# Kernel optimization log

Hardware: AMD Instinct MI355X
Metric: run time of the kernel (lower is better)

## Reference

```python
import jax, jax.numpy as jnp
import numpy as np

N_NODES = 100000


def _gcn_norm(edge_index, num_nodes):
    # Add self-loops, then symmetric normalization D^-1/2 A D^-1/2 (PyG gcn_norm).
    loops = jnp.arange(num_nodes, dtype=edge_index.dtype)
    src = jnp.concatenate([edge_index[0], loops])
    dst = jnp.concatenate([edge_index[1], loops])
    ew = jnp.ones(src.shape[0], dtype=jnp.float32)
    deg = jax.ops.segment_sum(ew, dst, num_segments=num_nodes)
    dinv = jnp.where(deg > 0, jax.lax.rsqrt(deg), 0.0)
    norm = dinv[src] * ew * dinv[dst]
    return src, dst, norm


def _prop_gcn_conv(x, W, b, src, dst, norm, num_nodes, prop_nums):
    # PropGCNConv: linear transform once, then prop_nums hops of normalized
    # sparse propagation (gather from src, scale, scatter-add to dst), + bias.
    x = x @ W
    for _ in range(prop_nums):
        msgs = x[src] * norm[:, None]              # [E, d]
        x = jax.ops.segment_sum(msgs, dst, num_segments=num_nodes)
    return x + b


def setup_inputs() -> dict:
    key = jax.random.key(0)
    k1, k2, k3, k4 = jax.random.split(key, 4)
    in_dim, hid_dim, num_classes = 128, 64, 40
    n_edges = 800000
    x = jax.random.normal(k1, (N_NODES, in_dim), dtype=jnp.float32)
    W0 = jax.random.normal(k2, (in_dim, hid_dim), dtype=jnp.float32) * (1.0 / np.sqrt(in_dim))
    b0 = jnp.zeros((hid_dim,), dtype=jnp.float32)
    Wc = jax.random.normal(k3, (hid_dim, num_classes), dtype=jnp.float32) * (1.0 / np.sqrt(hid_dim))
    bc = jnp.zeros((num_classes,), dtype=jnp.float32)
    edge_index = jax.random.randint(k4, (2, n_edges), 0, N_NODES, dtype=jnp.int64)
    return {"x": x, "W0": W0, "b0": b0, "Wc": Wc, "bc": bc,
            "edge_index": edge_index, "prop_nums": 30}


def reference(x, W0, b0, Wc, bc, edge_index, prop_nums):
    n = x.shape[0]
    src, dst, norm = _gcn_norm(edge_index, n)
    # feat_bottleneck: conv -> relu -> dropout (eval mode -> identity)
    h = _prop_gcn_conv(x, W0, b0, src, dst, norm, n, prop_nums)
    h = jax.nn.relu(h)
    # feat_classifier: single-hop PropGCNConv
    out = _prop_gcn_conv(h, Wc, bc, src, dst, norm, n, 1)
    return out
```

## Files before the change

### kernel.cpp

```cpp
#include <hip/hip_runtime.h>

#define NN  100000
#define NE  800000
#define NNZ 900000
#define IN_DIM 128
#define HID 64
#define NC  40
#define HOPS 30

typedef _Float16 half8 __attribute__((ext_vector_type(8)));


__global__ void count_edges_k(const int* __restrict__ dst, int* __restrict__ cnt) {
    int e = blockIdx.x * blockDim.x + threadIdx.x;
    if (e < NE) atomicAdd(&cnt[dst[e]], 1);
}

__global__ void dinv_k(const int* __restrict__ cnt, float* __restrict__ dinv) {
    int i = blockIdx.x * blockDim.x + threadIdx.x;
    if (i < NN) dinv[i] = rsqrtf((float)(cnt[i] + 1));
}

__global__ void scan_blocks_k(const int* __restrict__ cnt, int* __restrict__ rp,
                              int* __restrict__ partials) {
    __shared__ int s[256];
    int tid = threadIdx.x;
    int i = blockIdx.x * 256 + tid;
    int v = (i < NN) ? (cnt[i] + 1) : 0;
    s[tid] = v;
    __syncthreads();
    for (int off = 1; off < 256; off <<= 1) {
        int t = (tid >= off) ? s[tid - off] : 0;
        __syncthreads();
        s[tid] += t;
        __syncthreads();
    }
    if (i < NN) rp[i] = s[tid] - v;
    if (tid == 255) partials[blockIdx.x] = s[255];
}

__global__ void scan_partials_k(int* __restrict__ partials, int nblk) {
    __shared__ int s[512];
    int tid = threadIdx.x;
    int v = (tid < nblk) ? partials[tid] : 0;
    s[tid] = v;
    __syncthreads();
    for (int off = 1; off < 512; off <<= 1) {
        int t = (tid >= off) ? s[tid - off] : 0;
        __syncthreads();
        s[tid] += t;
        __syncthreads();
    }
    if (tid < nblk) partials[tid] = s[tid] - v;
}

__global__ void add_offsets_k(int* __restrict__ rp, const int* __restrict__ partials) {
    int i = blockIdx.x * 256 + threadIdx.x;
    if (i < NN) rp[i] += partials[blockIdx.x];
    if (i == 0) rp[NN] = NNZ;
}

__global__ void fill_csr_k(const int* __restrict__ src, const int* __restrict__ dst,
                           const float* __restrict__ dinv, const int* __restrict__ rp,
                           int* __restrict__ cnt, int2* __restrict__ cv) {
    int e = blockIdx.x * blockDim.x + threadIdx.x;
    if (e >= NNZ) return;
    int pos;
    int2 p;
    if (e < NE) {
        int s = src[e], d = dst[e];
        int old = atomicAdd(&cnt[d], -1);
        pos = rp[d] + old - 1;
        p.x = s;
        p.y = __float_as_int(dinv[s] * dinv[d]);
    } else {
        int i = e - NE;
        pos = rp[i + 1] - 1;
        p.x = i;
        p.y = __float_as_int(dinv[i] * dinv[i]);
    }
    cv[pos] = p;
}


__global__ void __launch_bounds__(256) gemm1_k(const float* __restrict__ x,
                                               const float* __restrict__ W,
                                               _Float16* __restrict__ out) {
    int t = threadIdx.x;
    int cq = __builtin_amdgcn_readfirstlane(t >> 6);
    int node = blockIdx.x * 64 + (t & 63);
    int nc = node < NN ? node : NN - 1;
    const float4* xr = (const float4*)(x + (size_t)nc * IN_DIM);
    const float* Wq = W + cq * 16;
    float acc[16];
#pragma unroll
    for (int c = 0; c < 16; ++c) acc[c] = 0.f;
#pragma unroll 4
    for (int k4 = 0; k4 < IN_DIM / 4; ++k4) {
        float4 xv = xr[k4];
#pragma unroll
        for (int kk = 0; kk < 4; ++kk) {
            float xs = (kk == 0) ? xv.x : (kk == 1) ? xv.y : (kk == 2) ? xv.z : xv.w;
            const float4* wr = (const float4*)(Wq + (k4 * 4 + kk) * HID);
#pragma unroll
            for (int c4 = 0; c4 < 4; ++c4) {
                float4 wv = wr[c4];
                acc[c4 * 4 + 0] = fmaf(xs, wv.x, acc[c4 * 4 + 0]);
                acc[c4 * 4 + 1] = fmaf(xs, wv.y, acc[c4 * 4 + 1]);
                acc[c4 * 4 + 2] = fmaf(xs, wv.z, acc[c4 * 4 + 2]);
                acc[c4 * 4 + 3] = fmaf(xs, wv.w, acc[c4 * 4 + 3]);
            }
        }
    }
    if (node < NN) {
        half8* o = (half8*)(out + (size_t)node * HID + cq * 16);
        half8 r0, r1;
#pragma unroll
        for (int j = 0; j < 8; ++j) {
            r0[j] = (_Float16)acc[j];
            r1[j] = (_Float16)acc[j + 8];
        }
        o[0] = r0;
        o[1] = r1;
    }
}

__global__ void prop64_k(const _Float16* __restrict__ xin, _Float16* __restrict__ xout,
                         const int* __restrict__ rp, const int2* __restrict__ cv) {
    int wid  = threadIdx.x >> 6;
    int lane = threadIdx.x & 63;
    int n    = lane >> 5;
    int s    = (lane >> 3) & 3;
    int f    = lane & 7;
    int node = blockIdx.x * 8 + wid * 2 + n;
    int beg = rp[node], end = rp[node + 1];
    const half8* x8 = (const half8*)xin;
    float a0 = 0.f, a1 = 0.f, a2 = 0.f, a3 = 0.f, a4 = 0.f, a5 = 0.f, a6 = 0.f, a7 = 0.f;
    for (int e = beg + s; e < end; e += 16) {
        int  e1 = e + 4,  e2 = e + 8,  e3 = e + 12;
        bool p1 = e1 < end, p2 = e2 < end, p3 = e3 < end;
        int2 q0 = cv[e];
        int2 q1 = cv[p1 ? e1 : beg];
        int2 q2 = cv[p2 ? e2 : beg];
        int2 q3 = cv[p3 ? e3 : beg];
        float v0 = __int_as_float(q0.y);
        float v1 = p1 ? __int_as_float(q1.y) : 0.f;
        float v2 = p2 ? __int_as_float(q2.y) : 0.f;
        float v3 = p3 ? __int_as_float(q3.y) : 0.f;
        half8 x0 = x8[(size_t)q0.x * 8 + f];
        half8 x1 = x8[(size_t)q1.x * 8 + f];
        half8 x2 = x8[(size_t)q2.x * 8 + f];
        half8 x3 = x8[(size_t)q3.x * 8 + f];
        a0 += v0 * (float)x0[0] + v1 * (float)x1[0] + v2 * (float)x2[0] + v3 * (float)x3[0];
        a1 += v0 * (float)x0[1] + v1 * (float)x1[1] + v2 * (float)x2[1] + v3 * (float)x3[1];
        a2 += v0 * (float)x0[2] + v1 * (float)x1[2] + v2 * (float)x2[2] + v3 * (float)x3[2];
        a3 += v0 * (float)x0[3] + v1 * (float)x1[3] + v2 * (float)x2[3] + v3 * (float)x3[3];
        a4 += v0 * (float)x0[4] + v1 * (float)x1[4] + v2 * (float)x2[4] + v3 * (float)x3[4];
        a5 += v0 * (float)x0[5] + v1 * (float)x1[5] + v2 * (float)x2[5] + v3 * (float)x3[5];
        a6 += v0 * (float)x0[6] + v1 * (float)x1[6] + v2 * (float)x2[6] + v3 * (float)x3[6];
        a7 += v0 * (float)x0[7] + v1 * (float)x1[7] + v2 * (float)x2[7] + v3 * (float)x3[7];
    }
#pragma unroll
    for (int m = 8; m <= 16; m <<= 1) {
        a0 += __shfl_xor(a0, m); a1 += __shfl_xor(a1, m);
        a2 += __shfl_xor(a2, m); a3 += __shfl_xor(a3, m);
        a4 += __shfl_xor(a4, m); a5 += __shfl_xor(a5, m);
        a6 += __shfl_xor(a6, m); a7 += __shfl_xor(a7, m);
    }
    if (s == 0) {
        half8 r;
        r[0] = (_Float16)a0; r[1] = (_Float16)a1; r[2] = (_Float16)a2; r[3] = (_Float16)a3;
        r[4] = (_Float16)a4; r[5] = (_Float16)a5; r[6] = (_Float16)a6; r[7] = (_Float16)a7;
        ((half8*)xout)[(size_t)node * 8 + f] = r;
    }
}

__global__ void __launch_bounds__(256, 4) gemm2_k(const _Float16* __restrict__ h,
                                                  const float* __restrict__ b0,
                                                  const float* __restrict__ Wc,
                                                  _Float16* __restrict__ g) {
    __shared__ float Wcs[HID * NC];
    __shared__ float b0s[HID];
    int t = threadIdx.x;
    for (int i = t; i < HID * NC / 4; i += 256)
        ((float4*)Wcs)[i] = ((const float4*)Wc)[i];
    if (t < HID) b0s[t] = b0[t];
    __syncthreads();
    int node = blockIdx.x * 256 + t;
    if (node >= NN) return;
    const half8* hr = (const half8*)(h + (size_t)node * HID);
    float acc[NC];
#pragma unroll
    for (int c = 0; c < NC; ++c) acc[c] = 0.f;
#pragma unroll
    for (int j = 0; j < 8; ++j) {
        half8 hv = hr[j];
#pragma unroll
        for (int m = 0; m < 8; ++m) {
            int k = j * 8 + m;
            float fv = fmaxf((float)hv[m] + b0s[k], 0.f);
            const float4* wr = (const float4*)(Wcs + k * NC);
#pragma unroll
            for (int c4 = 0; c4 < NC / 4; ++c4) {
                float4 wv = wr[c4];
                acc[c4 * 4 + 0] = fmaf(fv, wv.x, acc[c4 * 4 + 0]);
                acc[c4 * 4 + 1] = fmaf(fv, wv.y, acc[c4 * 4 + 1]);
                acc[c4 * 4 + 2] = fmaf(fv, wv.z, acc[c4 * 4 + 2]);
                acc[c4 * 4 + 3] = fmaf(fv, wv.w, acc[c4 * 4 + 3]);
            }
        }
    }
    half8* go = (half8*)(g + (size_t)node * NC);
#pragma unroll
    for (int j = 0; j < 5; ++j) {
        half8 r;
#pragma unroll
        for (int m = 0; m < 8; ++m) r[m] = (_Float16)acc[j * 8 + m];
        go[j] = r;
    }
}

__global__ void prop40_k(const _Float16* __restrict__ g, float* __restrict__ out,
                         const int* __restrict__ rp, const int2* __restrict__ cv,
                         const float* __restrict__ bc) {
    int t = blockIdx.x * 256 + threadIdx.x;
    int node = t >> 6;
    int lane = threadIdx.x & 63;
    int s = lane >> 3;
    int f = lane & 7;
    int beg = rp[node], end = rp[node + 1];
    const half8* g8 = (const half8*)g;
    bool act = f < 5;
    float a0 = 0.f, a1 = 0.f, a2 = 0.f, a3 = 0.f, a4 = 0.f, a5 = 0.f, a6 = 0.f, a7 = 0.f;
    for (int e = beg + s; e < end; e += 16) {
        int  e1 = e + 8;
        bool p1 = e1 < end;
        int2 q0 = cv[e];
        int2 q1 = cv[p1 ? e1 : beg];
        float v0 = __int_as_float(q0.y);
        float v1 = p1 ? __int_as_float(q1.y) : 0.f;
        if (act) {
            half8 x0 = g8[(size_t)q0.x * 5 + f];
            half8 x1 = g8[(size_t)q1.x * 5 + f];
            a0 += v0 * (float)x0[0] + v1 * (float)x1[0];
            a1 += v0 * (float)x0[1] + v1 * (float)x1[1];
            a2 += v0 * (float)x0[2] + v1 * (float)x1[2];
            a3 += v0 * (float)x0[3] + v1 * (float)x1[3];
            a4 += v0 * (float)x0[4] + v1 * (float)x1[4];
            a5 += v0 * (float)x0[5] + v1 * (float)x1[5];
            a6 += v0 * (float)x0[6] + v1 * (float)x1[6];
            a7 += v0 * (float)x0[7] + v1 * (float)x1[7];
        }
    }
#pragma unroll
    for (int m = 8; m <= 32; m <<= 1) {
        a0 += __shfl_xor(a0, m); a1 += __shfl_xor(a1, m);
        a2 += __shfl_xor(a2, m); a3 += __shfl_xor(a3, m);
        a4 += __shfl_xor(a4, m); a5 += __shfl_xor(a5, m);
        a6 += __shfl_xor(a6, m); a7 += __shfl_xor(a7, m);
    }
    if (s == 0 && act) {
        float* o = out + (size_t)node * NC + f * 8;
        o[0] = a0 + bc[f * 8 + 0];
        o[1] = a1 + bc[f * 8 + 1];
        o[2] = a2 + bc[f * 8 + 2];
        o[3] = a3 + bc[f * 8 + 3];
        o[4] = a4 + bc[f * 8 + 4];
        o[5] = a5 + bc[f * 8 + 5];
        o[6] = a6 + bc[f * 8 + 6];
        o[7] = a7 + bc[f * 8 + 7];
    }
}


extern "C" void kernel_launch(void* const* d_in, const int* in_sizes, int n_in,
                              void* d_out, int out_size, void* d_ws, size_t ws_size,
                              hipStream_t stream) {
    const float* x  = (const float*)d_in[0];
    const float* W0 = (const float*)d_in[1];
    const float* b0 = (const float*)d_in[2];
    const float* Wc = (const float*)d_in[3];
    const float* bc = (const float*)d_in[4];
    const int*   ei = (const int*)d_in[5];
    const int* src = ei;
    const int* dst = ei + NE;

    char* ws = (char*)d_ws;
    size_t off = 0;
    auto alloc = [&](size_t bytes) -> void* {
        void* p = ws + off;
        off = (off + bytes + 255) & ~(size_t)255;
        return p;
    };
    float* dinv     = (float*)alloc((size_t)NN * 4);
    int*   rp       = (int*)  alloc((size_t)(NN + 1) * 4);
    int*   cnt      = (int*)  alloc((size_t)NN * 4);
    int*   partials = (int*)  alloc(512 * 4);
    int2*  cvp      = (int2*) alloc((size_t)NNZ * 8);
    _Float16* XA    = (_Float16*)alloc((size_t)NN * HID * 2);
    _Float16* XB    = (_Float16*)alloc((size_t)NN * HID * 2);
    _Float16* G     = (_Float16*)alloc((size_t)NN * NC * 2);

    const int nblk_n = (NN + 255) / 256;

    hipMemsetAsync(cnt, 0, (size_t)NN * 4, stream);
    count_edges_k<<<(NE + 255) / 256, 256, 0, stream>>>(dst, cnt);
    dinv_k       <<<nblk_n, 256, 0, stream>>>(cnt, dinv);
    scan_blocks_k<<<nblk_n, 256, 0, stream>>>(cnt, rp, partials);
    scan_partials_k<<<1, 512, 0, stream>>>(partials, nblk_n);
    add_offsets_k<<<nblk_n, 256, 0, stream>>>(rp, partials);
    fill_csr_k   <<<(NNZ + 255) / 256, 256, 0, stream>>>(src, dst, dinv, rp, cnt, cvp);

    gemm1_k<<<(NN + 63) / 64, 256, 0, stream>>>(x, W0, XA);

    _Float16* a = XA;
    _Float16* b = XB;
    for (int hop = 0; hop < HOPS; ++hop) {
        prop64_k<<<NN / 8, 256, 0, stream>>>(a, b, rp, cvp);
        _Float16* tmp = a; a = b; b = tmp;
    }

    gemm2_k<<<nblk_n, 256, 0, stream>>>(a, b0, Wc, G);
    prop40_k<<<NN * HID / 256, 256, 0, stream>>>(G, (float*)d_out, rp, cvp, bc);
}
```

Baseline: 829.9 us.

## Split features into 16-wide slabs and fold GCN norm into per-node scales

Features are now stored as four column slabs of 16 halves each, with every slab contiguous over all nodes. The propagation kernel gathers from one slab per block, so the working set of each gather is about a quarter of the full feature matrix and fits more easily in cache. The symmetric normalization is rewritten as a pre-scale by D^-1/2, then unweighted neighbor sums rescaled by 1/deg each hop, with D^-1/2 on the final hop. This lets the CSR store only column indices instead of (index, weight) pairs. Nontemporal loads and stores and a block-index swizzle are also added. The trade-offs are more launched blocks that each re-read the row pointers and indices per slab, and a different rounding path in fp16.

```diff
diff --git a/kernel.cpp b/kernel.cpp
--- a/kernel.cpp
+++ b/kernel.cpp
@@ -7,6 +7,8 @@
 #define HID 64
 #define NC  40
 #define HOPS 30
+#define QF  16
+#define PROP_GRID (8 * 1563)
 
 typedef _Float16 half8 __attribute__((ext_vector_type(8)));
 
@@ -16,9 +18,15 @@
     if (e < NE) atomicAdd(&cnt[dst[e]], 1);
 }
 
-__global__ void dinv_k(const int* __restrict__ cnt, float* __restrict__ dinv) {
+__global__ void dinv_k(const int* __restrict__ cnt, float* __restrict__ dinv,
+                       float* __restrict__ dinv2) {
     int i = blockIdx.x * blockDim.x + threadIdx.x;
-    if (i < NN) dinv[i] = rsqrtf((float)(cnt[i] + 1));
+    if (i < NN) {
+        float deg = (float)(cnt[i] + 1);
+        float dv = rsqrtf(deg);
+        dinv[i] = dv;
+        dinv2[i] = 1.0f / deg;
+    }
 }
 
 __global__ void scan_blocks_k(const int* __restrict__ cnt, int* __restrict__ rp,
@@ -61,30 +69,24 @@
 }
 
 __global__ void fill_csr_k(const int* __restrict__ src, const int* __restrict__ dst,
-                           const float* __restrict__ dinv, const int* __restrict__ rp,
-                           int* __restrict__ cnt, int2* __restrict__ cv) {
+                           const int* __restrict__ rp, int* __restrict__ cnt,
+                           int* __restrict__ col) {
     int e = blockIdx.x * blockDim.x + threadIdx.x;
     if (e >= NNZ) return;
-    int pos;
-    int2 p;
     if (e < NE) {
-        int s = src[e], d = dst[e];
+        int d = dst[e];
         int old = atomicAdd(&cnt[d], -1);
-        pos = rp[d] + old - 1;
-        p.x = s;
-        p.y = __float_as_int(dinv[s] * dinv[d]);
+        col[rp[d] + old - 1] = src[e];
     } else {
         int i = e - NE;
-        pos = rp[i + 1] - 1;
-        p.x = i;
-        p.y = __float_as_int(dinv[i] * dinv[i]);
-    }
-    cv[pos] = p;
+        col[rp[i + 1] - 1] = i;
+    }
 }
 
 
 __global__ void __launch_bounds__(256) gemm1_k(const float* __restrict__ x,
                                                const float* __restrict__ W,
+                                               const float* __restrict__ dinv,
                                                _Float16* __restrict__ out) {
     int t = threadIdx.x;
     int cq = __builtin_amdgcn_readfirstlane(t >> 6);
@@ -113,65 +115,72 @@
         }
     }
     if (node < NN) {
-        half8* o = (half8*)(out + (size_t)node * HID + cq * 16);
+        float dv = dinv[node];
+        half8* o = (half8*)out + ((size_t)cq * NN + node) * 2;
         half8 r0, r1;
 #pragma unroll
         for (int j = 0; j < 8; ++j) {
-            r0[j] = (_Float16)acc[j];
-            r1[j] = (_Float16)acc[j + 8];
+            r0[j] = (_Float16)(acc[j] * dv);
+            r1[j] = (_Float16)(acc[j + 8] * dv);
         }
         o[0] = r0;
         o[1] = r1;
     }
 }
 
-__global__ void prop64_k(const _Float16* __restrict__ xin, _Float16* __restrict__ xout,
-                         const int* __restrict__ rp, const int2* __restrict__ cv) {
+__global__ void __launch_bounds__(256) prop16_k(const _Float16* __restrict__ yin,
+                                                _Float16* __restrict__ yout,
+                                                const int* __restrict__ rp,
+                                                const int* __restrict__ col,
+                                                const float* __restrict__ wsc) {
+    int b = blockIdx.x;
+    int q = (b & 7) >> 1;
+    int g = ((b >> 3) << 1) | (b & 1);
     int wid  = threadIdx.x >> 6;
     int lane = threadIdx.x & 63;
-    int n    = lane >> 5;
-    int s    = (lane >> 3) & 3;
-    int f    = lane & 7;
-    int node = blockIdx.x * 8 + wid * 2 + n;
-    int beg = rp[node], end = rp[node + 1];
-    const half8* x8 = (const half8*)xin;
-    float a0 = 0.f, a1 = 0.f, a2 = 0.f, a3 = 0.f, a4 = 0.f, a5 = 0.f, a6 = 0.f, a7 = 0.f;
-    for (int e = beg + s; e < end; e += 16) {
-        int  e1 = e + 4,  e2 = e + 8,  e3 = e + 12;
-        bool p1 = e1 < end, p2 = e2 < end, p3 = e3 < end;
-        int2 q0 = cv[e];
-        int2 q1 = cv[p1 ? e1 : beg];
-        int2 q2 = cv[p2 ? e2 : beg];
-        int2 q3 = cv[p3 ? e3 : beg];
-        float v0 = __int_as_float(q0.y);
-        float v1 = p1 ? __int_as_float(q1.y) : 0.f;
-        float v2 = p2 ? __int_as_float(q2.y) : 0.f;
-        float v3 = p3 ? __int_as_float(q3.y) : 0.f;
-        half8 x0 = x8[(size_t)q0.x * 8 + f];
-        half8 x1 = x8[(size_t)q1.x * 8 + f];
-        half8 x2 = x8[(size_t)q2.x * 8 + f];
-        half8 x3 = x8[(size_t)q3.x * 8 + f];
-        a0 += v0 * (float)x0[0] + v1 * (float)x1[0] + v2 * (float)x2[0] + v3 * (float)x3[0];
-        a1 += v0 * (float)x0[1] + v1 * (float)x1[1] + v2 * (float)x2[1] + v3 * (float)x3[1];
-        a2 += v0 * (float)x0[2] + v1 * (float)x1[2] + v2 * (float)x2[2] + v3 * (float)x3[2];
-        a3 += v0 * (float)x0[3] + v1 * (float)x1[3] + v2 * (float)x2[3] + v3 * (float)x3[3];
-        a4 += v0 * (float)x0[4] + v1 * (float)x1[4] + v2 * (float)x2[4] + v3 * (float)x3[4];
-        a5 += v0 * (float)x0[5] + v1 * (float)x1[5] + v2 * (float)x2[5] + v3 * (float)x3[5];
-        a6 += v0 * (float)x0[6] + v1 * (float)x1[6] + v2 * (float)x2[6] + v3 * (float)x3[6];
-        a7 += v0 * (float)x0[7] + v1 * (float)x1[7] + v2 * (float)x2[7] + v3 * (float)x3[7];
-    }
-#pragma unroll
-    for (int m = 8; m <= 16; m <<= 1) {
+    int n = lane >> 3;
+    int s = (lane >> 1) & 3;
+    int f = lane & 1;
+    int node = g * 32 + wid * 8 + n;
+    if (node >= NN) node = NN - 1;
+    int beg = __builtin_nontemporal_load(rp + node);
+    int end = __builtin_nontemporal_load(rp + node + 1);
+    const half8* x8 = (const half8*)yin + (size_t)q * NN * 2;
+    float a0 = 0.f, a1 = 0.f, a2 = 0.f, a3 = 0.f,
+          a4 = 0.f, a5 = 0.f, a6 = 0.f, a7 = 0.f;
+    for (int e = beg + s; e < end; e += 8) {
+        int  e1 = e + 4;
+        bool p1 = e1 < end;
+        int c0 = __builtin_nontemporal_load(col + e);
+        int c1 = __builtin_nontemporal_load(col + (p1 ? e1 : e));
+        float w1 = p1 ? 1.f : 0.f;
+        half8 xa = x8[c0 * 2 + f];
+        half8 xb = x8[c1 * 2 + f];
+        a0 += (float)xa[0]; a0 = fmaf(w1, (float)xb[0], a0);
+        a1 += (float)xa[1]; a1 = fmaf(w1, (float)xb[1], a1);
+        a2 += (float)xa[2]; a2 = fmaf(w1, (float)xb[2], a2);
+        a3 += (float)xa[3]; a3 = fmaf(w1, (float)xb[3], a3);
+        a4 += (float)xa[4]; a4 = fmaf(w1, (float)xb[4], a4);
+        a5 += (float)xa[5]; a5 = fmaf(w1, (float)xb[5], a5);
+        a6 += (float)xa[6]; a6 = fmaf(w1, (float)xb[6], a6);
+        a7 += (float)xa[7]; a7 = fmaf(w1, (float)xb[7], a7);
+    }
+#pragma unroll
+    for (int m = 2; m <= 4; m <<= 1) {
         a0 += __shfl_xor(a0, m); a1 += __shfl_xor(a1, m);
         a2 += __shfl_xor(a2, m); a3 += __shfl_xor(a3, m);
         a4 += __shfl_xor(a4, m); a5 += __shfl_xor(a5, m);
         a6 += __shfl_xor(a6, m); a7 += __shfl_xor(a7, m);
     }
     if (s == 0) {
+        float sc = wsc[node];
         half8 r;
-        r[0] = (_Float16)a0; r[1] = (_Float16)a1; r[2] = (_Float16)a2; r[3] = (_Float16)a3;
-        r[4] = (_Float16)a4; r[5] = (_Float16)a5; r[6] = (_Float16)a6; r[7] = (_Float16)a7;
-        ((half8*)xout)[(size_t)node * 8 + f] = r;
+        r[0] = (_Float16)(a0 * sc); r[1] = (_Float16)(a1 * sc);
+        r[2] = (_Float16)(a2 * sc); r[3] = (_Float16)(a3 * sc);
+        r[4] = (_Float16)(a4 * sc); r[5] = (_Float16)(a5 * sc);
+        r[6] = (_Float16)(a6 * sc); r[7] = (_Float16)(a7 * sc);
+        half8* o8 = (half8*)yout + (size_t)q * NN * 2;
+        __builtin_nontemporal_store(r, &o8[(size_t)node * 2 + f]);
     }
 }
 
@@ -188,25 +197,28 @@
     __syncthreads();
     int node = blockIdx.x * 256 + t;
     if (node >= NN) return;
-    const half8* hr = (const half8*)(h + (size_t)node * HID);
+    const half8* hq = (const half8*)h;
     float acc[NC];
 #pragma unroll
     for (int c = 0; c < NC; ++c) acc[c] = 0.f;
 #pragma unroll
-    for (int j = 0; j < 8; ++j) {
-        half8 hv = hr[j];
-#pragma unroll
-        for (int m = 0; m < 8; ++m) {
-            int k = j * 8 + m;
-            float fv = fmaxf((float)hv[m] + b0s[k], 0.f);
-            const float4* wr = (const float4*)(Wcs + k * NC);
-#pragma unroll
-            for (int c4 = 0; c4 < NC / 4; ++c4) {
-                float4 wv = wr[c4];
-                acc[c4 * 4 + 0] = fmaf(fv, wv.x, acc[c4 * 4 + 0]);
-                acc[c4 * 4 + 1] = fmaf(fv, wv.y, acc[c4 * 4 + 1]);
-                acc[c4 * 4 + 2] = fmaf(fv, wv.z, acc[c4 * 4 + 2]);
-                acc[c4 * 4 + 3] = fmaf(fv, wv.w, acc[c4 * 4 + 3]);
+    for (int q = 0; q < 4; ++q) {
+#pragma unroll
+        for (int jj = 0; jj < 2; ++jj) {
+            half8 hv = hq[((size_t)q * NN + node) * 2 + jj];
+#pragma unroll
+            for (int m = 0; m < 8; ++m) {
+                int k = q * 16 + jj * 8 + m;
+                float fv = fmaxf((float)hv[m] + b0s[k], 0.f);
+                const float4* wr = (const float4*)(Wcs + k * NC);
+#pragma unroll
+                for (int c4 = 0; c4 < NC / 4; ++c4) {
+                    float4 wv = wr[c4];
+                    acc[c4 * 4 + 0] = fmaf(fv, wv.x, acc[c4 * 4 + 0]);
+                    acc[c4 * 4 + 1] = fmaf(fv, wv.y, acc[c4 * 4 + 1]);
+                    acc[c4 * 4 + 2] = fmaf(fv, wv.z, acc[c4 * 4 + 2]);
+                    acc[c4 * 4 + 3] = fmaf(fv, wv.w, acc[c4 * 4 + 3]);
+                }
             }
         }
     }
@@ -221,27 +233,28 @@
 }
 
 __global__ void prop40_k(const _Float16* __restrict__ g, float* __restrict__ out,
-                         const int* __restrict__ rp, const int2* __restrict__ cv,
-                         const float* __restrict__ bc) {
+                         const int* __restrict__ rp, const int* __restrict__ col,
+                         const float* __restrict__ dinv, const float* __restrict__ bc) {
     int t = blockIdx.x * 256 + threadIdx.x;
     int node = t >> 6;
     int lane = threadIdx.x & 63;
     int s = lane >> 3;
     int f = lane & 7;
     int beg = rp[node], end = rp[node + 1];
+    float dd = dinv[node];
     const half8* g8 = (const half8*)g;
     bool act = f < 5;
     float a0 = 0.f, a1 = 0.f, a2 = 0.f, a3 = 0.f, a4 = 0.f, a5 = 0.f, a6 = 0.f, a7 = 0.f;
     for (int e = beg + s; e < end; e += 16) {
         int  e1 = e + 8;
         bool p1 = e1 < end;
-        int2 q0 = cv[e];
-        int2 q1 = cv[p1 ? e1 : beg];
-        float v0 = __int_as_float(q0.y);
-        float v1 = p1 ? __int_as_float(q1.y) : 0.f;
+        int c0 = col[e];
+        int c1 = col[p1 ? e1 : e];
+        float v0 = dinv[c0] * dd;
+        float v1 = p1 ? dinv[c1] * dd : 0.f;
         if (act) {
-            half8 x0 = g8[(size_t)q0.x * 5 + f];
-            half8 x1 = g8[(size_t)q1.x * 5 + f];
+            half8 x0 = g8[(size_t)c0 * 5 + f];
+            half8 x1 = g8[(size_t)c1 * 5 + f];
             a0 += v0 * (float)x0[0] + v1 * (float)x1[0];
             a1 += v0 * (float)x0[1] + v1 * (float)x1[1];
             a2 += v0 * (float)x0[2] + v1 * (float)x1[2];
@@ -293,33 +306,35 @@
         return p;
     };
     float* dinv     = (float*)alloc((size_t)NN * 4);
+    float* dinv2    = (float*)alloc((size_t)NN * 4);
     int*   rp       = (int*)  alloc((size_t)(NN + 1) * 4);
     int*   cnt      = (int*)  alloc((size_t)NN * 4);
     int*   partials = (int*)  alloc(512 * 4);
-    int2*  cvp      = (int2*) alloc((size_t)NNZ * 8);
-    _Float16* XA    = (_Float16*)alloc((size_t)NN * HID * 2);
-    _Float16* XB    = (_Float16*)alloc((size_t)NN * HID * 2);
+    int*   col      = (int*)  alloc((size_t)NNZ * 4);
+    _Float16* YA    = (_Float16*)alloc((size_t)NN * HID * 2);
+    _Float16* YB    = (_Float16*)alloc((size_t)NN * HID * 2);
     _Float16* G     = (_Float16*)alloc((size_t)NN * NC * 2);
 
     const int nblk_n = (NN + 255) / 256;
 
     hipMemsetAsync(cnt, 0, (size_t)NN * 4, stream);
     count_edges_k<<<(NE + 255) / 256, 256, 0, stream>>>(dst, cnt);
-    dinv_k       <<<nblk_n, 256, 0, stream>>>(cnt, dinv);
+    dinv_k       <<<nblk_n, 256, 0, stream>>>(cnt, dinv, dinv2);
     scan_blocks_k<<<nblk_n, 256, 0, stream>>>(cnt, rp, partials);
     scan_partials_k<<<1, 512, 0, stream>>>(partials, nblk_n);
     add_offsets_k<<<nblk_n, 256, 0, stream>>>(rp, partials);
-    fill_csr_k   <<<(NNZ + 255) / 256, 256, 0, stream>>>(src, dst, dinv, rp, cnt, cvp);
-
-    gemm1_k<<<(NN + 63) / 64, 256, 0, stream>>>(x, W0, XA);
-
-    _Float16* a = XA;
-    _Float16* b = XB;
+    fill_csr_k   <<<(NNZ + 255) / 256, 256, 0, stream>>>(src, dst, rp, cnt, col);
+
+    gemm1_k<<<(NN + 63) / 64, 256, 0, stream>>>(x, W0, dinv, YA);
+
+    _Float16* a = YA;
+    _Float16* b = YB;
     for (int hop = 0; hop < HOPS; ++hop) {
-        prop64_k<<<NN / 8, 256, 0, stream>>>(a, b, rp, cvp);
+        const float* wsc = (hop == HOPS - 1) ? dinv : dinv2;
+        prop16_k<<<PROP_GRID, 256, 0, stream>>>(a, b, rp, col, wsc);
         _Float16* tmp = a; a = b; b = tmp;
     }
 
-    gemm2_k<<<nblk_n, 256, 0, stream>>>(a, b0, Wc, G);
-    prop40_k<<<NN * HID / 256, 256, 0, stream>>>(G, (float*)d_out, rp, cvp, bc);
-}
+    gemm2_k<<<nblk_n, 256, 0, stream>>>(YA, b0, Wc, G);
+    prop40_k<<<NN * HID / 256, 256, 0, stream>>>(G, (float*)d_out, rp, col, dinv, bc);
+}
```

Measured after the change: 1.408 ms. 1.7x slower.

## Handle self-loops analytically in propagation and split gemm2 columns across waves

Applied to the files above, without the earlier changes.

Self-loop entries are removed from the CSR. Each node's own term (dinv^2 * x[node]) is added in the epilogue of the propagation kernels, which shrinks the edge list and the gathers inside the loop. The padding index for inactive lanes now points at the current edge instead of the row start. gemm2 is rearranged so four waves each compute 10 of the 40 output columns for 64 nodes, which cuts registers per thread and lifts the launch-bounds occupancy hint. In exchange, every output node does one extra contiguous row load in the epilogue.

```diff
diff --git a/kernel.cpp b/kernel.cpp
--- a/kernel.cpp
+++ b/kernel.cpp
@@ -2,7 +2,6 @@
 
 #define NN  100000
 #define NE  800000
-#define NNZ 900000
 #define IN_DIM 128
 #define HID 64
 #define NC  40
@@ -26,7 +25,7 @@
     __shared__ int s[256];
     int tid = threadIdx.x;
     int i = blockIdx.x * 256 + tid;
-    int v = (i < NN) ? (cnt[i] + 1) : 0;
+    int v = (i < NN) ? cnt[i] : 0;
     s[tid] = v;
     __syncthreads();
     for (int off = 1; off < 256; off <<= 1) {
@@ -57,29 +56,20 @@
 __global__ void add_offsets_k(int* __restrict__ rp, const int* __restrict__ partials) {
     int i = blockIdx.x * 256 + threadIdx.x;
     if (i < NN) rp[i] += partials[blockIdx.x];
-    if (i == 0) rp[NN] = NNZ;
+    if (i == 0) rp[NN] = NE;
 }
 
 __global__ void fill_csr_k(const int* __restrict__ src, const int* __restrict__ dst,
                            const float* __restrict__ dinv, const int* __restrict__ rp,
                            int* __restrict__ cnt, int2* __restrict__ cv) {
     int e = blockIdx.x * blockDim.x + threadIdx.x;
-    if (e >= NNZ) return;
-    int pos;
+    if (e >= NE) return;
+    int s = src[e], d = dst[e];
+    int old = atomicAdd(&cnt[d], -1);
     int2 p;
-    if (e < NE) {
-        int s = src[e], d = dst[e];
-        int old = atomicAdd(&cnt[d], -1);
-        pos = rp[d] + old - 1;
-        p.x = s;
-        p.y = __float_as_int(dinv[s] * dinv[d]);
-    } else {
-        int i = e - NE;
-        pos = rp[i + 1] - 1;
-        p.x = i;
-        p.y = __float_as_int(dinv[i] * dinv[i]);
-    }
-    cv[pos] = p;
+    p.x = s;
+    p.y = __float_as_int(dinv[s] * dinv[d]);
+    cv[rp[d] + old - 1] = p;
 }
 
 
@@ -126,7 +116,8 @@
 }
 
 __global__ void prop64_k(const _Float16* __restrict__ xin, _Float16* __restrict__ xout,
-                         const int* __restrict__ rp, const int2* __restrict__ cv) {
+                         const int* __restrict__ rp, const int2* __restrict__ cv,
+                         const float* __restrict__ dinv) {
     int wid  = threadIdx.x >> 6;
     int lane = threadIdx.x & 63;
     int n    = lane >> 5;
@@ -140,9 +131,9 @@
         int  e1 = e + 4,  e2 = e + 8,  e3 = e + 12;
         bool p1 = e1 < end, p2 = e2 < end, p3 = e3 < end;
         int2 q0 = cv[e];
-        int2 q1 = cv[p1 ? e1 : beg];
-        int2 q2 = cv[p2 ? e2 : beg];
-        int2 q3 = cv[p3 ? e3 : beg];
+        int2 q1 = cv[p1 ? e1 : e];
+        int2 q2 = cv[p2 ? e2 : e];
+        int2 q3 = cv[p3 ? e3 : e];
         float v0 = __int_as_float(q0.y);
         float v1 = p1 ? __int_as_float(q1.y) : 0.f;
         float v2 = p2 ? __int_as_float(q2.y) : 0.f;
@@ -168,17 +159,26 @@
         a6 += __shfl_xor(a6, m); a7 += __shfl_xor(a7, m);
     }
     if (s == 0) {
+        float dv = dinv[node];
+        float w = dv * dv;
+        half8 xo = x8[(size_t)node * 8 + f];
         half8 r;
-        r[0] = (_Float16)a0; r[1] = (_Float16)a1; r[2] = (_Float16)a2; r[3] = (_Float16)a3;
-        r[4] = (_Float16)a4; r[5] = (_Float16)a5; r[6] = (_Float16)a6; r[7] = (_Float16)a7;
+        r[0] = (_Float16)(a0 + w * (float)xo[0]);
+        r[1] = (_Float16)(a1 + w * (float)xo[1]);
+        r[2] = (_Float16)(a2 + w * (float)xo[2]);
+        r[3] = (_Float16)(a3 + w * (float)xo[3]);
+        r[4] = (_Float16)(a4 + w * (float)xo[4]);
+        r[5] = (_Float16)(a5 + w * (float)xo[5]);
+        r[6] = (_Float16)(a6 + w * (float)xo[6]);
+        r[7] = (_Float16)(a7 + w * (float)xo[7]);
         ((half8*)xout)[(size_t)node * 8 + f] = r;
     }
 }
 
-__global__ void __launch_bounds__(256, 4) gemm2_k(const _Float16* __restrict__ h,
-                                                  const float* __restrict__ b0,
-                                                  const float* __restrict__ Wc,
-                                                  _Float16* __restrict__ g) {
+__global__ void __launch_bounds__(256) gemm2_k(const _Float16* __restrict__ h,
+                                               const float* __restrict__ b0,
+                                               const float* __restrict__ Wc,
+                                               _Float16* __restrict__ g) {
     __shared__ float Wcs[HID * NC];
     __shared__ float b0s[HID];
     int t = threadIdx.x;
@@ -186,12 +186,13 @@
         ((float4*)Wcs)[i] = ((const float4*)Wc)[i];
     if (t < HID) b0s[t] = b0[t];
     __syncthreads();
-    int node = blockIdx.x * 256 + t;
+    int cq = __builtin_amdgcn_readfirstlane(t >> 6);
+    int node = blockIdx.x * 64 + (t & 63);
     if (node >= NN) return;
     const half8* hr = (const half8*)(h + (size_t)node * HID);
-    float acc[NC];
-#pragma unroll
-    for (int c = 0; c < NC; ++c) acc[c] = 0.f;
+    float acc[10];
+#pragma unroll
+    for (int c = 0; c < 10; ++c) acc[c] = 0.f;
 #pragma unroll
     for (int j = 0; j < 8; ++j) {
         half8 hv = hr[j];
@@ -199,30 +200,25 @@
         for (int m = 0; m < 8; ++m) {
             int k = j * 8 + m;
             float fv = fmaxf((float)hv[m] + b0s[k], 0.f);
-            const float4* wr = (const float4*)(Wcs + k * NC);
-#pragma unroll
-            for (int c4 = 0; c4 < NC / 4; ++c4) {
-                float4 wv = wr[c4];
-                acc[c4 * 4 + 0] = fmaf(fv, wv.x, acc[c4 * 4 + 0]);
-                acc[c4 * 4 + 1] = fmaf(fv, wv.y, acc[c4 * 4 + 1]);
-                acc[c4 * 4 + 2] = fmaf(fv, wv.z, acc[c4 * 4 + 2]);
-                acc[c4 * 4 + 3] = fmaf(fv, wv.w, acc[c4 * 4 + 3]);
-            }
+            const float* wr = Wcs + k * NC + cq * 10;
+#pragma unroll
+            for (int c = 0; c < 10; ++c)
+                acc[c] = fmaf(fv, wr[c], acc[c]);
         }
     }
-    half8* go = (half8*)(g + (size_t)node * NC);
-#pragma unroll
-    for (int j = 0; j < 5; ++j) {
-        half8 r;
-#pragma unroll
-        for (int m = 0; m < 8; ++m) r[m] = (_Float16)acc[j * 8 + m];
-        go[j] = r;
+    unsigned* go = (unsigned*)((char*)g + (size_t)node * 80 + cq * 20);
+#pragma unroll
+    for (int i = 0; i < 5; ++i) {
+        union { _Float16 hh[2]; unsigned u; } u;
+        u.hh[0] = (_Float16)acc[2 * i];
+        u.hh[1] = (_Float16)acc[2 * i + 1];
+        go[i] = u.u;
     }
 }
 
 __global__ void prop40_k(const _Float16* __restrict__ g, float* __restrict__ out,
                          const int* __restrict__ rp, const int2* __restrict__ cv,
-                         const float* __restrict__ bc) {
+                         const float* __restrict__ dinv, const float* __restrict__ bc) {
     int t = blockIdx.x * 256 + threadIdx.x;
     int node = t >> 6;
     int lane = threadIdx.x & 63;
@@ -236,7 +232,7 @@
         int  e1 = e + 8;
         bool p1 = e1 < end;
         int2 q0 = cv[e];
-        int2 q1 = cv[p1 ? e1 : beg];
+        int2 q1 = cv[p1 ? e1 : e];
         float v0 = __int_as_float(q0.y);
         float v1 = p1 ? __int_as_float(q1.y) : 0.f;
         if (act) {
@@ -260,15 +256,18 @@
         a6 += __shfl_xor(a6, m); a7 += __shfl_xor(a7, m);
     }
     if (s == 0 && act) {
+        float dv = dinv[node];
+        float w = dv * dv;
+        half8 xo = g8[(size_t)node * 5 + f];
         float* o = out + (size_t)node * NC + f * 8;
-        o[0] = a0 + bc[f * 8 + 0];
-        o[1] = a1 + bc[f * 8 + 1];
-        o[2] = a2 + bc[f * 8 + 2];
-        o[3] = a3 + bc[f * 8 + 3];
-        o[4] = a4 + bc[f * 8 + 4];
-        o[5] = a5 + bc[f * 8 + 5];
-        o[6] = a6 + bc[f * 8 + 6];
-        o[7] = a7 + bc[f * 8 + 7];
+        o[0] = a0 + w * (float)xo[0] + bc[f * 8 + 0];
+        o[1] = a1 + w * (float)xo[1] + bc[f * 8 + 1];
+        o[2] = a2 + w * (float)xo[2] + bc[f * 8 + 2];
+        o[3] = a3 + w * (float)xo[3] + bc[f * 8 + 3];
+        o[4] = a4 + w * (float)xo[4] + bc[f * 8 + 4];
+        o[5] = a5 + w * (float)xo[5] + bc[f * 8 + 5];
+        o[6] = a6 + w * (float)xo[6] + bc[f * 8 + 6];
+        o[7] = a7 + w * (float)xo[7] + bc[f * 8 + 7];
     }
 }
 
@@ -296,12 +295,13 @@
     int*   rp       = (int*)  alloc((size_t)(NN + 1) * 4);
     int*   cnt      = (int*)  alloc((size_t)NN * 4);
     int*   partials = (int*)  alloc(512 * 4);
-    int2*  cvp      = (int2*) alloc((size_t)NNZ * 8);
+    int2*  cvp      = (int2*) alloc((size_t)NE * 8);
     _Float16* XA    = (_Float16*)alloc((size_t)NN * HID * 2);
     _Float16* XB    = (_Float16*)alloc((size_t)NN * HID * 2);
     _Float16* G     = (_Float16*)alloc((size_t)NN * NC * 2);
 
     const int nblk_n = (NN + 255) / 256;
+    const int nblk64 = (NN + 63) / 64;
 
     hipMemsetAsync(cnt, 0, (size_t)NN * 4, stream);
     count_edges_k<<<(NE + 255) / 256, 256, 0, stream>>>(dst, cnt);
@@ -309,17 +309,17 @@
     scan_blocks_k<<<nblk_n, 256, 0, stream>>>(cnt, rp, partials);
     scan_partials_k<<<1, 512, 0, stream>>>(partials, nblk_n);
     add_offsets_k<<<nblk_n, 256, 0, stream>>>(rp, partials);
-    fill_csr_k   <<<(NNZ + 255) / 256, 256, 0, stream>>>(src, dst, dinv, rp, cnt, cvp);
-
-    gemm1_k<<<(NN + 63) / 64, 256, 0, stream>>>(x, W0, XA);
+    fill_csr_k   <<<(NE + 255) / 256, 256, 0, stream>>>(src, dst, dinv, rp, cnt, cvp);
+
+    gemm1_k<<<nblk64, 256, 0, stream>>>(x, W0, XA);
 
     _Float16* a = XA;
     _Float16* b = XB;
     for (int hop = 0; hop < HOPS; ++hop) {
-        prop64_k<<<NN / 8, 256, 0, stream>>>(a, b, rp, cvp);
+        prop64_k<<<NN / 8, 256, 0, stream>>>(a, b, rp, cvp, dinv);
         _Float16* tmp = a; a = b; b = tmp;
     }
 
-    gemm2_k<<<nblk_n, 256, 0, stream>>>(a, b0, Wc, G);
-    prop40_k<<<NN * HID / 256, 256, 0, stream>>>(G, (float*)d_out, rp, cvp, bc);
-}
+    gemm2_k<<<nblk64, 256, 0, stream>>>(a, b0, Wc, G);
+    prop40_k<<<NN * HID / 256, 256, 0, stream>>>(G, (float*)d_out, rp, cvp, dinv, bc);
+}
```

Measured after the change: 893.3 us. 1.08x slower.
